# Kernel tuning notes

Measured on AMD Instinct MI355X. Metric: run time of the kernel, lower is better.

## Reference

```python
import jax, jax.numpy as jnp
import numpy as np

N = 100000   # nodes
E = 1600000  # edges
D = 128      # in_dim == hidden_dim
EL = 100000  # label edges for decode


def setup_inputs() -> dict:
    key = jax.random.key(0)
    k1, k2, k3, k4, k5 = jax.random.split(key, 5)
    x = jax.random.normal(k1, (N, D), dtype=jnp.float32)
    edge_index = jax.random.randint(k2, (2, E), 0, N, dtype=jnp.int64)
    edge_label_index = jax.random.randint(k3, (2, EL), 0, N, dtype=jnp.int64)
    # Glorot-ish init for GCN weights
    scale = 1.0 / np.sqrt(D)
    W1 = jax.random.normal(k4, (D, D), dtype=jnp.float32) * scale
    W2 = jax.random.normal(k5, (D, D), dtype=jnp.float32) * scale
    b1 = jnp.zeros((D,), dtype=jnp.float32)
    b2 = jnp.zeros((D,), dtype=jnp.float32)
    return {"x": x, "edge_index": edge_index, "edge_label_index": edge_label_index,
            "W1": W1, "b1": b1, "W2": W2, "b2": b2}


def gcn_conv(x, src, dst, W, b, num_nodes):
    # PyG GCNConv: add self-loops, symmetric D^-1/2 A D^-1/2 normalization
    loop = jnp.arange(num_nodes, dtype=src.dtype)
    s = jnp.concatenate([src, loop])
    d = jnp.concatenate([dst, loop])
    deg = jax.ops.segment_sum(jnp.ones(d.shape, dtype=x.dtype), d, num_segments=num_nodes)
    dinv = jnp.where(deg > 0, jax.lax.rsqrt(jnp.maximum(deg, 1.0)), 0.0)
    norm = dinv[s] * dinv[d]                      # [E+N]
    h = x @ W                                     # [N, H]
    msg = h[s] * norm[:, None]                    # gather + scale
    out = jax.ops.segment_sum(msg, d, num_segments=num_nodes)  # scatter-add
    return out + b


def reference(x, edge_index, edge_label_index, W1, b1, W2, b2):
    src, dst = edge_index[0], edge_index[1]
    z = jax.nn.relu(gcn_conv(x, src, dst, W1, b1, N))
    z = jax.nn.relu(gcn_conv(z, src, dst, W2, b2, N))
    # decode: edge-wise dot product
    s, d = edge_label_index[0], edge_label_index[1]
    return jnp.sum(z[s] * z[d], axis=-1)          # [EL]
```

## Files before the change

kernel.cpp:

```cpp
#include <hip/hip_runtime.h>
#include <hip/hip_bf16.h>
#include <hip/hip_fp16.h>


typedef _Float16 half8 __attribute__((ext_vector_type(8)));
typedef float floatx4 __attribute__((ext_vector_type(4)));

#define BK_SHIFT 8
#define BSC_EDGES 2048
#define SLAB_CAP 5120
#define WPAD 136

__global__ __launch_bounds__(256) void k_bin(const int* __restrict__ src,
                                             const int* __restrict__ dst,
                                             int* __restrict__ bins,
                                             int* __restrict__ P,
                                             int E, int nbk, int nbin,
                                             const float* __restrict__ W1,
                                             const float* __restrict__ W2,
                                             _Float16* __restrict__ WT1,
                                             _Float16* __restrict__ WT2) {
    int tid = threadIdx.x;
    if ((int)blockIdx.x >= nbin) {
        int b2 = blockIdx.x - nbin;
        if (tid < 128) {
            const float* W = (b2 < 128) ? W1 : W2;
            _Float16* WT = (b2 < 128) ? WT1 : WT2;
            int k = b2 & 127;
            WT[tid * 128 + k] = (_Float16)W[k * 128 + tid];
        }
        return;
    }

    __shared__ int lcnt[1024];
    __shared__ int delta[1024];
    __shared__ int ssum[256];
    __shared__ int stage[BSC_EDGES];
    int e0 = blockIdx.x * BSC_EDGES;
    int nloc = E - e0; if (nloc > BSC_EDGES) nloc = BSC_EDGES;

    for (int b = tid; b < nbk; b += 256) lcnt[b] = 0;
    __syncthreads();

    int d[BSC_EDGES / 256], s[BSC_EDGES / 256];
#pragma unroll
    for (int k = 0; k < BSC_EDGES / 256; ++k) {
        int e = e0 + k * 256 + tid;
        if (e < E) {
            d[k] = dst[e];
            s[k] = src[e];
            atomicAdd(&lcnt[d[k] >> BK_SHIFT], 1);
        } else d[k] = -1;
    }
    __syncthreads();

    const int gpb = (nbk + 255) >> 8;
    int c[4], mysum = 0;
    for (int t = 0; t < gpb; ++t) {
        int b = tid * gpb + t;
        c[t] = (b < nbk) ? lcnt[b] : 0;
        mysum += c[t];
    }
    ssum[tid] = mysum;
    __syncthreads();
    for (int off = 1; off < 256; off <<= 1) {
        int t = (tid >= off) ? ssum[tid - off] : 0;
        __syncthreads();
        ssum[tid] += t;
        __syncthreads();
    }
    int base = ssum[tid] - mysum;
    for (int t = 0; t < gpb; ++t) {
        int b = tid * gpb + t;
        if (b < nbk) {
            delta[b] = base;
            lcnt[b] = base;
            base += c[t];
        }
    }
    __syncthreads();

#pragma unroll
    for (int k = 0; k < BSC_EDGES / 256; ++k) {
        if (d[k] >= 0) {
            int b = d[k] >> BK_SHIFT;
            int lp = atomicAdd(&lcnt[b], 1);
            stage[lp] = (s[k] << 8) | (d[k] & 255);
        }
    }
    __syncthreads();

    int* bb = bins + (size_t)blockIdx.x * BSC_EDGES;
    for (int j = tid; j < nloc; j += 256) bb[j] = stage[j];
    int prow = nbk + 1;
    int* pp = P + (size_t)blockIdx.x * prow;
    for (int b = tid; b <= nbk; b += 256)
        pp[b] = (b < nbk) ? delta[b] : nloc;
}

template <typename AT>
__global__ __launch_bounds__(256) void k_csr_gemm(const int* __restrict__ bins,
                                                  const int* __restrict__ P,
                                                  int* __restrict__ row_start,
                                                  int* __restrict__ cnt,
                                                  float* __restrict__ dinv,
                                                  int* __restrict__ srcs,
                                                  const AT* __restrict__ X,
                                                  const _Float16* __restrict__ WT,
                                                  _Float16* __restrict__ G,
                                                  int n, int nbk, int nbin) {
    __shared__ __align__(16) char smem[128 * WPAD * 2];
    int tid = threadIdx.x;

    if ((int)blockIdx.x < nbk) {
        int* stage = (int*)smem;
        int* lcnt  = (int*)(smem + 20480);
        int* lpos  = (int*)(smem + 21504);
        int* curs  = (int*)(smem + 22528);
        int b = blockIdx.x;
        int prow = nbk + 1;
        if (tid == 0) *curs = 0;
        __syncthreads();
        for (int seg = tid; seg < nbin; seg += 256) {
            const int* pp = P + (size_t)seg * prow + b;
            int p0 = pp[0], p1 = pp[1];
            int len = p1 - p0;
            if (len > 0) {
                int off = atomicAdd(curs, len);
                const int* sp = bins + (size_t)seg * BSC_EDGES + p0;
                for (int i = 0; i < len; ++i) stage[off + i] = sp[i];
            }
        }
        __syncthreads();
        int tot = *curs;
        lcnt[tid] = 0;
        __syncthreads();
        for (int i = tid; i < tot; i += 256)
            atomicAdd(&lcnt[stage[i] & 255], 1);
        __syncthreads();
        int c = lcnt[tid];
        lpos[tid] = c;
        __syncthreads();
        for (int off = 1; off < 256; off <<= 1) {
            int t = (tid >= off) ? lpos[tid - off] : 0;
            __syncthreads();
            lpos[tid] += t;
            __syncthreads();
        }
        int rs = b * SLAB_CAP + lpos[tid] - c;
        int v = (b << BK_SHIFT) + tid;
        if (v < n) {
            row_start[v] = rs;
            cnt[v] = c;
            dinv[v] = rsqrtf((float)c + 1.0f);
        }
        __syncthreads();
        lpos[tid] = rs;
        __syncthreads();
        for (int i = tid; i < tot; i += 256) {
            int p = stage[i];
            int loc = atomicAdd(&lpos[p & 255], 1);
            srcs[loc] = p >> 8;
        }
        return;
    }

    _Float16* Wl = (_Float16*)smem;
    {
        const half8* w8 = (const half8*)WT;
#pragma unroll
        for (int i = 0; i < 8; ++i) {
            int idx = i * 256 + tid;
            int r = idx >> 4, cc = idx & 15;
            *(half8*)(Wl + r * WPAD + cc * 8) = w8[idx];
        }
    }
    __syncthreads();

    auto loadA = [](const AT* p) -> half8 {
        if constexpr (sizeof(AT) == 4) {
            const float4* f = (const float4*)p;
            float4 f0 = f[0], f1 = f[1];
            half8 a;
            a[0] = (_Float16)f0.x; a[1] = (_Float16)f0.y;
            a[2] = (_Float16)f0.z; a[3] = (_Float16)f0.w;
            a[4] = (_Float16)f1.x; a[5] = (_Float16)f1.y;
            a[6] = (_Float16)f1.z; a[7] = (_Float16)f1.w;
            return a;
        } else {
            return *(const half8*)p;
        }
    };

    int bid = blockIdx.x - nbk;
    int wave = tid >> 6, lane = tid & 63;
    int q = lane >> 4, ln = lane & 15;
    int m0 = bid * 128 + wave * 32;
    int mA0 = m0 + ln;      if (mA0 >= n) mA0 = n - 1;
    int mA1 = m0 + 16 + ln; if (mA1 >= n) mA1 = n - 1;
    const AT* xr0 = X + (size_t)mA0 * 128;
    const AT* xr1 = X + (size_t)mA1 * 128;

    floatx4 acc[2][8];
#pragma unroll
    for (int p = 0; p < 2; ++p)
#pragma unroll
        for (int t = 0; t < 8; ++t) acc[p][t] = (floatx4){0.f, 0.f, 0.f, 0.f};

#pragma unroll
    for (int kc = 0; kc < 128; kc += 32) {
        half8 a0 = loadA(xr0 + kc + q * 8);
        half8 a1 = loadA(xr1 + kc + q * 8);
#pragma unroll
        for (int t = 0; t < 8; ++t) {
            half8 b = *(const half8*)(Wl + (size_t)(t * 16 + ln) * WPAD + kc + q * 8);
            acc[0][t] = __builtin_amdgcn_mfma_f32_16x16x32_f16(a0, b, acc[0][t], 0, 0, 0);
            acc[1][t] = __builtin_amdgcn_mfma_f32_16x16x32_f16(a1, b, acc[1][t], 0, 0, 0);
        }
    }

#pragma unroll
    for (int p = 0; p < 2; ++p) {
#pragma unroll
        for (int r = 0; r < 4; ++r) {
            int row = m0 + p * 16 + q * 4 + r;
            if (row < n) {
                _Float16* grow = G + (size_t)row * 128 + ln;
#pragma unroll
                for (int t = 0; t < 8; ++t)
                    grow[t * 16] = (_Float16)acc[p][t][r];
            }
        }
    }
}

template <typename AT>
__global__ __launch_bounds__(256) void k_gemm_mfma(const AT* __restrict__ X,
                                                   const _Float16* __restrict__ WT,
                                                   _Float16* __restrict__ G, int n) {
    __shared__ _Float16 Wl[128 * WPAD];
    int tid = threadIdx.x;
    {
        const half8* w8 = (const half8*)WT;
#pragma unroll
        for (int i = 0; i < 8; ++i) {
            int idx = i * 256 + tid;
            int r = idx >> 4, cc = idx & 15;
            *(half8*)(Wl + r * WPAD + cc * 8) = w8[idx];
        }
    }
    __syncthreads();

    auto loadA = [](const AT* p) -> half8 {
        if constexpr (sizeof(AT) == 4) {
            const float4* f = (const float4*)p;
            float4 f0 = f[0], f1 = f[1];
            half8 a;
            a[0] = (_Float16)f0.x; a[1] = (_Float16)f0.y;
            a[2] = (_Float16)f0.z; a[3] = (_Float16)f0.w;
            a[4] = (_Float16)f1.x; a[5] = (_Float16)f1.y;
            a[6] = (_Float16)f1.z; a[7] = (_Float16)f1.w;
            return a;
        } else {
            return *(const half8*)p;
        }
    };

    int wave = tid >> 6, lane = tid & 63;
    int q = lane >> 4, ln = lane & 15;
    int m0 = blockIdx.x * 128 + wave * 32;
    int mA0 = m0 + ln;      if (mA0 >= n) mA0 = n - 1;
    int mA1 = m0 + 16 + ln; if (mA1 >= n) mA1 = n - 1;
    const AT* xr0 = X + (size_t)mA0 * 128;
    const AT* xr1 = X + (size_t)mA1 * 128;

    floatx4 acc[2][8];
#pragma unroll
    for (int p = 0; p < 2; ++p)
#pragma unroll
        for (int t = 0; t < 8; ++t) acc[p][t] = (floatx4){0.f, 0.f, 0.f, 0.f};

#pragma unroll
    for (int kc = 0; kc < 128; kc += 32) {
        half8 a0 = loadA(xr0 + kc + q * 8);
        half8 a1 = loadA(xr1 + kc + q * 8);
#pragma unroll
        for (int t = 0; t < 8; ++t) {
            half8 b = *(const half8*)(Wl + (size_t)(t * 16 + ln) * WPAD + kc + q * 8);
            acc[0][t] = __builtin_amdgcn_mfma_f32_16x16x32_f16(a0, b, acc[0][t], 0, 0, 0);
            acc[1][t] = __builtin_amdgcn_mfma_f32_16x16x32_f16(a1, b, acc[1][t], 0, 0, 0);
        }
    }

#pragma unroll
    for (int p = 0; p < 2; ++p) {
#pragma unroll
        for (int r = 0; r < 4; ++r) {
            int row = m0 + p * 16 + q * 4 + r;
            if (row < n) {
                _Float16* grow = G + (size_t)row * 128 + ln;
#pragma unroll
                for (int t = 0; t < 8; ++t)
                    grow[t * 16] = (_Float16)acc[p][t][r];
            }
        }
    }
}

__global__ __launch_bounds__(256) void k_gather_relu(const _Float16* __restrict__ G,
                                                     const int* __restrict__ srcs,
                                                     const int* __restrict__ row_start,
                                                     const int* __restrict__ cnt,
                                                     const float* __restrict__ dinv,
                                                     const float* __restrict__ bias,
                                                     _Float16* __restrict__ Z, int n) {
    int v = blockIdx.x * 16 + (threadIdx.x >> 4);
    int lane = threadIdx.x & 15;
    if (v >= n) return;
    const half8* G8 = (const half8*)G;

    float dv = dinv[v];
    half8 self = G8[(size_t)v * 16 + lane];
    float acc[8], acc2[8];
#pragma unroll
    for (int j = 0; j < 8; ++j) { acc[j] = dv * (float)self[j]; acc2[j] = 0.f; }

    int beg = row_start[v], deg = cnt[v];
    int e = 0;
    for (; e + 3 < deg; e += 4) {
        int s0 = srcs[beg + e];
        int s1 = srcs[beg + e + 1];
        int s2 = srcs[beg + e + 2];
        int s3 = srcs[beg + e + 3];
        float d0 = dinv[s0];
        float d1 = dinv[s1];
        float d2 = dinv[s2];
        float d3 = dinv[s3];
        half8 t0 = G8[(size_t)s0 * 16 + lane];
        half8 t1 = G8[(size_t)s1 * 16 + lane];
        half8 t2 = G8[(size_t)s2 * 16 + lane];
        half8 t3 = G8[(size_t)s3 * 16 + lane];
#pragma unroll
        for (int j = 0; j < 8; ++j) {
            acc[j]  += d0 * (float)t0[j] + d1 * (float)t1[j];
            acc2[j] += d2 * (float)t2[j] + d3 * (float)t3[j];
        }
    }
    for (; e < deg; ++e) {
        int s0 = srcs[beg + e];
        float d0 = dinv[s0];
        half8 t0 = G8[(size_t)s0 * 16 + lane];
#pragma unroll
        for (int j = 0; j < 8; ++j) acc[j] += d0 * (float)t0[j];
    }

    const float4* b4 = (const float4*)bias;
    float4 bb0 = b4[lane * 2], bb1 = b4[lane * 2 + 1];
    float bf[8] = {bb0.x, bb0.y, bb0.z, bb0.w, bb1.x, bb1.y, bb1.z, bb1.w};
    half8 zo;
#pragma unroll
    for (int j = 0; j < 8; ++j) {
        float z = dv * (acc[j] + acc2[j]) + bf[j];
        zo[j] = (_Float16)fmaxf(z, 0.f);
    }
    ((half8*)Z)[(size_t)v * 16 + lane] = zo;
}

__global__ __launch_bounds__(256) void k_decode(const _Float16* __restrict__ Z,
                                                const int* __restrict__ eli,
                                                float* __restrict__ out, int el) {
    int sub = threadIdx.x >> 4, lane = threadIdx.x & 15;
    int e = blockIdx.x * 16 + sub;
    if (e >= el) return;
    int s = eli[e], d = eli[el + e];
    const half8* Z8 = (const half8*)Z;
    half8 a = Z8[(size_t)s * 16 + lane];
    half8 b = Z8[(size_t)d * 16 + lane];
    float dot = 0.f;
#pragma unroll
    for (int j = 0; j < 8; ++j) dot += (float)a[j] * (float)b[j];
#pragma unroll
    for (int off = 8; off; off >>= 1) dot += __shfl_down(dot, off, 16);
    if (lane == 0) out[e] = dot;
}

extern "C" void kernel_launch(void* const* d_in, const int* in_sizes, int n_in,
                              void* d_out, int out_size, void* d_ws, size_t ws_size,
                              hipStream_t stream) {
    const float* x  = (const float*)d_in[0];
    const int*  ei  = (const int*)d_in[1];
    const int*  eli = (const int*)d_in[2];
    const float* W1 = (const float*)d_in[3];
    const float* b1 = (const float*)d_in[4];
    const float* W2 = (const float*)d_in[5];
    const float* b2 = (const float*)d_in[6];
    float* out = (float*)d_out;

    const int N  = in_sizes[0] / 128;
    const int E  = in_sizes[1] / 2;
    const int EL = in_sizes[2] / 2;
    const int* src = ei;
    const int* dst = ei + E;
    const int NBK  = (N + 255) >> BK_SHIFT;
    const int NBIN = (E + BSC_EDGES - 1) / BSC_EDGES;
    const int GB   = (N + 127) / 128;

    char* ws = (char*)d_ws;
    size_t off = 0;
    auto alloc = [&](size_t bytes) -> void* {
        void* p = ws + off;
        off += bytes;
        off = (off + 255) & ~(size_t)255;
        return p;
    };
    int*       cnt       = (int*)alloc((size_t)N * 4);
    int*       row_start = (int*)alloc((size_t)N * 4);
    float*     dinv      = (float*)alloc((size_t)N * 4);
    _Float16*  WT1       = (_Float16*)alloc(128 * 128 * 2);
    _Float16*  WT2       = (_Float16*)alloc(128 * 128 * 2);
    int*       srcs      = (int*)alloc((size_t)NBK * SLAB_CAP * 4);
    int*       bins      = (int*)alloc((size_t)NBIN * BSC_EDGES * 4);
    int*       P         = (int*)alloc((size_t)NBIN * (NBK + 1) * 4);
    _Float16*  buf0      = (_Float16*)alloc((size_t)N * 128 * 2);
    _Float16*  buf1      = (_Float16*)alloc((size_t)N * 128 * 2);

    k_bin<<<NBIN + 256, 256, 0, stream>>>(src, dst, bins, P, E, NBK, NBIN,
                                          W1, W2, WT1, WT2);

    k_csr_gemm<float><<<NBK + GB, 256, 0, stream>>>(bins, P, row_start, cnt, dinv,
                                                    srcs, x, WT1, buf0, N, NBK, NBIN);

    k_gather_relu<<<(N + 15) / 16, 256, 0, stream>>>(buf0, srcs, row_start, cnt, dinv, b1, buf1, N);
    k_gemm_mfma<_Float16><<<GB, 256, 0, stream>>>(buf1, WT2, buf0, N);
    k_gather_relu<<<(N + 15) / 16, 256, 0, stream>>>(buf0, srcs, row_start, cnt, dinv, b2, buf1, N);
    k_decode<<<(EL + 15) / 16, 256, 0, stream>>>(buf1, eli, out, EL);
}
```

Baseline: 277.9 us.

## Interleave two bin segments per thread in CSR staging and split gather launches

In the CSR build phase each thread now handles two bin segments at once, interleaving their copies into the shared stage buffer to expose more memory-level parallelism per thread. Separately, each gather+ReLU pass is split into two launches covering the lower and upper halves of the nodes. The split launches add launch overhead on the same stream and give no overlap, since they run serially. The interleaved copy adds branches per iteration.

Measured after the change: 303.2 us. 9.1% more time.

```diff
diff --git a/kernel.cpp b/kernel.cpp
--- a/kernel.cpp
+++ b/kernel.cpp
@@ -121,14 +121,25 @@
         int prow = nbk + 1;
         if (tid == 0) *curs = 0;
         __syncthreads();
-        for (int seg = tid; seg < nbin; seg += 256) {
-            const int* pp = P + (size_t)seg * prow + b;
-            int p0 = pp[0], p1 = pp[1];
-            int len = p1 - p0;
-            if (len > 0) {
-                int off = atomicAdd(curs, len);
-                const int* sp = bins + (size_t)seg * BSC_EDGES + p0;
-                for (int i = 0; i < len; ++i) stage[off + i] = sp[i];
+        int half = (nbin + 1) >> 1;
+        for (int seg = tid; seg < half; seg += 256) {
+            const int* ppA = P + (size_t)seg * prow + b;
+            int a0 = ppA[0], a1 = ppA[1];
+            int segB = seg + half;
+            int b0 = 0, b1 = 0;
+            if (segB < nbin) {
+                const int* ppB = P + (size_t)segB * prow + b;
+                b0 = ppB[0]; b1 = ppB[1];
+            }
+            int lenA = a1 - a0, lenB = b1 - b0;
+            int offA = lenA > 0 ? atomicAdd(curs, lenA) : 0;
+            int offB = lenB > 0 ? atomicAdd(curs, lenB) : 0;
+            const int* spA = bins + (size_t)seg * BSC_EDGES + a0;
+            const int* spB = bins + (size_t)segB * BSC_EDGES + b0;
+            int m = lenA > lenB ? lenA : lenB;
+            for (int i = 0; i < m; ++i) {
+                if (i < lenA) stage[offA + i] = spA[i];
+                if (i < lenB) stage[offB + i] = spB[i];
             }
         }
         __syncthreads();
@@ -313,10 +324,11 @@
                                                      const int* __restrict__ cnt,
                                                      const float* __restrict__ dinv,
                                                      const float* __restrict__ bias,
-                                                     _Float16* __restrict__ Z, int n) {
-    int v = blockIdx.x * 16 + (threadIdx.x >> 4);
+                                                     _Float16* __restrict__ Z,
+                                                     int vbase, int vcnt) {
+    int v = vbase + blockIdx.x * 16 + (threadIdx.x >> 4);
     int lane = threadIdx.x & 15;
-    if (v >= n) return;
+    if (v >= vbase + vcnt) return;
     const half8* G8 = (const half8*)G;
 
     float dv = dinv[v];
@@ -424,14 +436,20 @@
     _Float16*  buf0      = (_Float16*)alloc((size_t)N * 128 * 2);
     _Float16*  buf1      = (_Float16*)alloc((size_t)N * 128 * 2);
 
+    const int NH = ((N / 2) + 15) & ~15;
+    const int G1 = (NH + 15) / 16;
+    const int G2 = (N - NH + 15) / 16;
+
     k_bin<<<NBIN + 256, 256, 0, stream>>>(src, dst, bins, P, E, NBK, NBIN,
                                           W1, W2, WT1, WT2);
 
     k_csr_gemm<float><<<NBK + GB, 256, 0, stream>>>(bins, P, row_start, cnt, dinv,
                                                     srcs, x, WT1, buf0, N, NBK, NBIN);
 
-    k_gather_relu<<<(N + 15) / 16, 256, 0, stream>>>(buf0, srcs, row_start, cnt, dinv, b1, buf1, N);
+    k_gather_relu<<<G1, 256, 0, stream>>>(buf0, srcs, row_start, cnt, dinv, b1, buf1, 0, NH);
+    k_gather_relu<<<G2, 256, 0, stream>>>(buf0, srcs, row_start, cnt, dinv, b1, buf1, NH, N - NH);
     k_gemm_mfma<_Float16><<<GB, 256, 0, stream>>>(buf1, WT2, buf0, N);
-    k_gather_relu<<<(N + 15) / 16, 256, 0, stream>>>(buf0, srcs, row_start, cnt, dinv, b2, buf1, N);
+    k_gather_relu<<<G1, 256, 0, stream>>>(buf0, srcs, row_start, cnt, dinv, b2, buf1, 0, NH);
+    k_gather_relu<<<G2, 256, 0, stream>>>(buf0, srcs, row_start, cnt, dinv, b2, buf1, NH, N - NH);
     k_decode<<<(EL + 15) / 16, 256, 0, stream>>>(buf1, eli, out, EL);
 }
```

## Enlarge binning chunks and gather bin segments with whole waves

Applied to the files above, without the earlier changes.

Each binning block now handles 16384 edges instead of 2048, so there are far fewer bins (about 98 instead of 782). Edges are re-read from global memory in a strided loop instead of being held in registers. In the CSR stage, each wave now copies one segment with its 64 lanes working together, where before a single thread copied a whole segment serially. This cuts how many segments each bucket must visit and makes those copies coalesced, at the cost of lower parallelism and a large 64KB shared stage in k_bin, which limits occupancy.

After: 306.7 us. 10.4% more time.

```diff
diff --git a/kernel.cpp b/kernel.cpp
--- a/kernel.cpp
+++ b/kernel.cpp
@@ -7,7 +7,7 @@
 typedef float floatx4 __attribute__((ext_vector_type(4)));
 
 #define BK_SHIFT 8
-#define BSC_EDGES 2048
+#define BIN_EDGES 16384
 #define SLAB_CAP 5120
 #define WPAD 136
 
@@ -35,23 +35,15 @@
     __shared__ int lcnt[1024];
     __shared__ int delta[1024];
     __shared__ int ssum[256];
-    __shared__ int stage[BSC_EDGES];
-    int e0 = blockIdx.x * BSC_EDGES;
-    int nloc = E - e0; if (nloc > BSC_EDGES) nloc = BSC_EDGES;
+    __shared__ int stage[BIN_EDGES];
+    int e0 = blockIdx.x * BIN_EDGES;
+    int nloc = E - e0; if (nloc > BIN_EDGES) nloc = BIN_EDGES;
 
     for (int b = tid; b < nbk; b += 256) lcnt[b] = 0;
     __syncthreads();
 
-    int d[BSC_EDGES / 256], s[BSC_EDGES / 256];
-#pragma unroll
-    for (int k = 0; k < BSC_EDGES / 256; ++k) {
-        int e = e0 + k * 256 + tid;
-        if (e < E) {
-            d[k] = dst[e];
-            s[k] = src[e];
-            atomicAdd(&lcnt[d[k] >> BK_SHIFT], 1);
-        } else d[k] = -1;
-    }
+    for (int j = tid; j < nloc; j += 256)
+        atomicAdd(&lcnt[dst[e0 + j] >> BK_SHIFT], 1);
     __syncthreads();
 
     const int gpb = (nbk + 255) >> 8;
@@ -80,17 +72,15 @@
     }
     __syncthreads();
 
-#pragma unroll
-    for (int k = 0; k < BSC_EDGES / 256; ++k) {
-        if (d[k] >= 0) {
-            int b = d[k] >> BK_SHIFT;
-            int lp = atomicAdd(&lcnt[b], 1);
-            stage[lp] = (s[k] << 8) | (d[k] & 255);
-        }
-    }
-    __syncthreads();
-
-    int* bb = bins + (size_t)blockIdx.x * BSC_EDGES;
+    for (int j = tid; j < nloc; j += 256) {
+        int d = dst[e0 + j];
+        int s = src[e0 + j];
+        int lp = atomicAdd(&lcnt[d >> BK_SHIFT], 1);
+        stage[lp] = (s << 8) | (d & 255);
+    }
+    __syncthreads();
+
+    int* bb = bins + (size_t)blockIdx.x * BIN_EDGES;
     for (int j = tid; j < nloc; j += 256) bb[j] = stage[j];
     int prow = nbk + 1;
     int* pp = P + (size_t)blockIdx.x * prow;
@@ -121,14 +111,18 @@
         int prow = nbk + 1;
         if (tid == 0) *curs = 0;
         __syncthreads();
-        for (int seg = tid; seg < nbin; seg += 256) {
+        int wave = tid >> 6, lane = tid & 63;
+        for (int seg = wave; seg < nbin; seg += 4) {
             const int* pp = P + (size_t)seg * prow + b;
             int p0 = pp[0], p1 = pp[1];
             int len = p1 - p0;
             if (len > 0) {
-                int off = atomicAdd(curs, len);
-                const int* sp = bins + (size_t)seg * BSC_EDGES + p0;
-                for (int i = 0; i < len; ++i) stage[off + i] = sp[i];
+                int off = 0;
+                if (lane == 0) off = atomicAdd(curs, len);
+                off = __shfl(off, 0, 64);
+                const int* sp = bins + (size_t)seg * BIN_EDGES + p0;
+                for (int i = lane; i < len; i += 64)
+                    stage[off + i] = sp[i];
             }
         }
         __syncthreads();
@@ -402,7 +396,7 @@
     const int* src = ei;
     const int* dst = ei + E;
     const int NBK  = (N + 255) >> BK_SHIFT;
-    const int NBIN = (E + BSC_EDGES - 1) / BSC_EDGES;
+    const int NBIN = (E + BIN_EDGES - 1) / BIN_EDGES;
     const int GB   = (N + 127) / 128;
 
     char* ws = (char*)d_ws;
@@ -419,7 +413,7 @@
     _Float16*  WT1       = (_Float16*)alloc(128 * 128 * 2);
     _Float16*  WT2       = (_Float16*)alloc(128 * 128 * 2);
     int*       srcs      = (int*)alloc((size_t)NBK * SLAB_CAP * 4);
-    int*       bins      = (int*)alloc((size_t)NBIN * BSC_EDGES * 4);
+    int*       bins      = (int*)alloc((size_t)NBIN * BIN_EDGES * 4);
     int*       P         = (int*)alloc((size_t)NBIN * (NBK + 1) * 4);
     _Float16*  buf0      = (_Float16*)alloc((size_t)N * 128 * 2);
     _Float16*  buf1      = (_Float16*)alloc((size_t)N * 128 * 2);
```
